# Optimization experiments

Measured on AMD Instinct MI355X. Metric: run time of the kernel, lower is better.

The kernel has to match this reference:

```python
import jax, jax.numpy as jnp
import numpy as np

N_NODES = 50000
N_EDGES = 800000
N_GRAPHS = 512
IN_DIM = 128
HIDDEN = 256
N_CLASSES = 10
MID = 12  # fixed inter-layer dim in TwoConvSAGE


def _segment_mean(x, ids, num_segments):
    s = jax.ops.segment_sum(x, ids, num_segments=num_segments)
    cnt = jax.ops.segment_sum(jnp.ones((x.shape[0],), x.dtype), ids, num_segments=num_segments)
    return jnp.where(cnt[:, None] > 0, s / jnp.maximum(cnt, 1.0)[:, None], 0.0)


def _sage_layer(h, src, dst, Wa, ba, Wb, bb):
    # copy_u + mean: mean over incoming edges of src features
    h_neigh = _segment_mean(h[src], dst, N_NODES)  # [N, d]
    h_total = jnp.concatenate([h, h_neigh], axis=1)  # [N, 2d]
    # nn.Sequential(Linear, Linear) has NO activation in between
    z = (h_total @ Wa + ba) @ Wb + bb
    return jax.nn.relu(z)  # inner F.relu; outer F.relu is idempotent


def setup_inputs() -> dict:
    key = jax.random.key(0)
    ks = jax.random.split(key, 16)
    d = {}
    d['h'] = jax.random.normal(ks[0], (N_NODES, IN_DIM), jnp.float32)
    d['src'] = jax.random.randint(ks[1], (N_EDGES,), 0, N_NODES, jnp.int32)
    d['dst'] = jax.random.randint(ks[2], (N_EDGES,), 0, N_NODES, jnp.int32)
    d['graph_id'] = jnp.sort(jax.random.randint(ks[3], (N_NODES,), 0, N_GRAPHS, jnp.int32))
    s1 = 1.0 / np.sqrt(2 * IN_DIM)
    d['W1a'] = jax.random.uniform(ks[4], (2 * IN_DIM, HIDDEN), jnp.float32, -s1, s1)
    d['b1a'] = jax.random.uniform(ks[5], (HIDDEN,), jnp.float32, -s1, s1)
    s2 = 1.0 / np.sqrt(HIDDEN)
    d['W1b'] = jax.random.uniform(ks[6], (HIDDEN, MID), jnp.float32, -s2, s2)
    d['b1b'] = jax.random.uniform(ks[7], (MID,), jnp.float32, -s2, s2)
    s3 = 1.0 / np.sqrt(2 * MID)
    d['W2a'] = jax.random.uniform(ks[8], (2 * MID, HIDDEN), jnp.float32, -s3, s3)
    d['b2a'] = jax.random.uniform(ks[9], (HIDDEN,), jnp.float32, -s3, s3)
    d['W2b'] = jax.random.uniform(ks[10], (HIDDEN, MID), jnp.float32, -s2, s2)
    d['b2b'] = jax.random.uniform(ks[11], (MID,), jnp.float32, -s2, s2)
    s4 = 1.0 / np.sqrt(MID)
    d['Wc'] = jax.random.uniform(ks[12], (MID, N_CLASSES), jnp.float32, -s4, s4)
    d['bc'] = jax.random.uniform(ks[13], (N_CLASSES,), jnp.float32, -s4, s4)
    return d


def reference(h, src, dst, graph_id, W1a, b1a, W1b, b1b, W2a, b2a, W2b, b2b, Wc, bc):
    h1 = _sage_layer(h, src, dst, W1a, b1a, W1b, b1b)   # [N, 12]
    h2 = _sage_layer(h1, src, dst, W2a, b2a, W2b, b2b)  # [N, 12]
    hg = _segment_mean(h2, graph_id, N_GRAPHS)          # [G, 12]
    return hg @ Wc + bc                                  # [G, n_classes]
```

## Files before the change

### kernel.cpp

```cpp
#include <hip/hip_runtime.h>
#include <hip/hip_bf16.h>

#define NN 50000
#define NE 800000
#define NG 512
#define NB 196
#define B1_CHUNK 2048
#define B1_BLOCKS ((NE + B1_CHUNK - 1) / B1_CHUNK)

typedef unsigned long long ull;

__global__ void prep_kernel(const int* __restrict__ dst, int* __restrict__ hist_mat,
                            const float* __restrict__ W1a, const float* __restrict__ b1a,
                            const float* __restrict__ W1b, const float* __restrict__ b1b,
                            const float* __restrict__ W2a, const float* __restrict__ b2a,
                            const float* __restrict__ W2b, const float* __restrict__ b2b,
                            float* __restrict__ W1eff, float* __restrict__ b1eff,
                            float* __restrict__ W2eff, float* __restrict__ b2eff,
                            const int* __restrict__ gid, int* __restrict__ gstart) {
    int bid = blockIdx.x;
    int tid = threadIdx.x;
    if (bid < B1_BLOCKS) {
        __shared__ int hist[NB];
        for (int i = tid; i < NB; i += 256) hist[i] = 0;
        __syncthreads();
        int e0 = bid * B1_CHUNK;
        #pragma unroll
        for (int k = 0; k < 8; ++k) {
            int e = e0 + tid + k * 256;
            if (e < NE) atomicAdd(&hist[dst[e] >> 8], 1);
        }
        __syncthreads();
        int* row = hist_mat + bid * NB;
        for (int i = tid; i < NB; i += 256) row[i] = hist[i];
    } else if (bid < B1_BLOCKS + 14) {
        int t = (bid - B1_BLOCKS) * 256 + tid;
        if (t < 3072) {
            int r = t / 12, c = t % 12;
            float acc = 0.f;
            for (int k = 0; k < 256; ++k) acc += W1a[r*256 + k] * W1b[k*12 + c];
            W1eff[r*12 + c] = acc;
        } else if (t < 3084) {
            int c = t - 3072;
            float acc = b1b[c];
            for (int k = 0; k < 256; ++k) acc += b1a[k] * W1b[k*12 + c];
            b1eff[c] = acc;
        } else if (t < 3372) {
            int u = t - 3084;
            int r = u / 12, c = u % 12;
            float acc = 0.f;
            for (int k = 0; k < 256; ++k) acc += W2a[r*256 + k] * W2b[k*12 + c];
            W2eff[r*12 + c] = acc;
        } else if (t < 3384) {
            int c = t - 3372;
            float acc = b2b[c];
            for (int k = 0; k < 256; ++k) acc += b2a[k] * W2b[k*12 + c];
            b2eff[c] = acc;
        }
    } else {
        int n = (bid - B1_BLOCKS - 14) * 256 + tid;
        if (n < NN) {
            int cur = gid[n];
            int prev = (n == 0) ? -1 : gid[n - 1];
            for (int g = prev + 1; g <= cur; ++g) gstart[g] = n;
            if (n == NN - 1) {
                for (int g = cur + 1; g <= NG; ++g) gstart[g] = NN;
            }
        }
    }
}

__global__ void offs_kernel(const int* __restrict__ hist_mat,
                            int* __restrict__ off_mat, int* __restrict__ btot) {
    __shared__ int sh[512];
    int tid = threadIdx.x;
    int b = blockIdx.x;
    int v = (tid < B1_BLOCKS) ? hist_mat[tid * NB + b] : 0;
    sh[tid] = v;
    __syncthreads();
    for (int off = 1; off < 512; off <<= 1) {
        int t = (tid >= off) ? sh[tid - off] : 0;
        __syncthreads();
        sh[tid] += t;
        __syncthreads();
    }
    if (tid < B1_BLOCKS) off_mat[tid * NB + b] = sh[tid] - v;
    if (tid == B1_BLOCKS - 1) btot[b] = sh[tid];
}

__global__ void place_pairs_kernel(const int* __restrict__ src, const int* __restrict__ dst,
                                   const int* __restrict__ off_mat, const int* __restrict__ btot,
                                   ull* __restrict__ pairs) {
    __shared__ int sb[256];
    __shared__ int lbase[NB];
    __shared__ int lcur[NB];
    int tid = threadIdx.x;
    int v = (tid < NB) ? btot[tid] : 0;
    sb[tid] = v;
    __syncthreads();
    for (int off = 1; off < 256; off <<= 1) {
        int t = (tid >= off) ? sb[tid - off] : 0;
        __syncthreads();
        sb[tid] += t;
        __syncthreads();
    }
    const int* orow = off_mat + blockIdx.x * NB;
    if (tid < NB) {
        lbase[tid] = (sb[tid] - v) + orow[tid];
        lcur[tid] = 0;
    }
    __syncthreads();
    int e0 = blockIdx.x * B1_CHUNK;
    #pragma unroll
    for (int k = 0; k < 8; ++k) {
        int e = e0 + tid + k * 256;
        if (e < NE) {
            int dd = dst[e];
            int ss = src[e];
            int bb = dd >> 8;
            int idx = atomicAdd(&lcur[bb], 1);
            pairs[lbase[bb] + idx] = ((ull)(unsigned)ss << 32) | (unsigned)dd;
        }
    }
}

__global__ void p1_kernel(const float* __restrict__ h, const float* __restrict__ W1eff,
                          float* __restrict__ p1t, float* __restrict__ p1b) {
    int n = blockIdx.x * blockDim.x + threadIdx.x;
    if (n >= NN) return;
    const float4* hrow = (const float4*)(h + (size_t)n * 128);
    float acc[24];
    #pragma unroll
    for (int j = 0; j < 24; ++j) acc[j] = 0.f;
    #pragma unroll 4
    for (int kq = 0; kq < 32; ++kq) {
        float4 hv = hrow[kq];
        #pragma unroll
        for (int u = 0; u < 4; ++u) {
            int k = kq * 4 + u;
            float hx = u == 0 ? hv.x : (u == 1 ? hv.y : (u == 2 ? hv.z : hv.w));
            const float4* wt = (const float4*)(W1eff + k * 12);
            const float4* wb = (const float4*)(W1eff + (128 + k) * 12);
            #pragma unroll
            for (int q = 0; q < 3; ++q) {
                float4 a = wt[q];
                float4 b = wb[q];
                acc[q*4 + 0]      += hx * a.x;
                acc[q*4 + 1]      += hx * a.y;
                acc[q*4 + 2]      += hx * a.z;
                acc[q*4 + 3]      += hx * a.w;
                acc[12 + q*4 + 0] += hx * b.x;
                acc[12 + q*4 + 1] += hx * b.y;
                acc[12 + q*4 + 2] += hx * b.z;
                acc[12 + q*4 + 3] += hx * b.w;
            }
        }
    }
    float* pt = p1t + (size_t)n * 12;
    float* pb = p1b + (size_t)n * 12;
    #pragma unroll
    for (int c = 0; c < 12; ++c) pt[c] = acc[c];
    #pragma unroll
    for (int c = 0; c < 12; ++c) pb[c] = acc[12 + c];
}

__global__ void fine_gf1_kernel(const ull* __restrict__ pairs, const int* __restrict__ btot,
                                const float* __restrict__ p1t, const float* __restrict__ p1b,
                                const float* __restrict__ b1eff, const float* __restrict__ W2eff,
                                int* __restrict__ row_start, int* __restrict__ sorted_src,
                                float* __restrict__ p2t, float* __restrict__ p2b) {
    __shared__ int sb[256];
    __shared__ int cnt[256];
    __shared__ int sc[256];
    __shared__ int rs[257];
    __shared__ float hacc[256 * 13];
    __shared__ float w2[288];
    __shared__ float b1[12];
    int tid = threadIdx.x;
    int b = blockIdx.x;
    if (tid < 256) { sb[tid] = (tid < NB) ? btot[tid] : 0; cnt[tid] = 0; }
    for (int i = tid; i < 288; i += 768) w2[i] = W2eff[i];
    if (tid >= 256 && tid < 268) b1[tid - 256] = b1eff[tid - 256];
    __syncthreads();
    for (int off = 1; off < 256; off <<= 1) {
        int t = (tid < 256 && tid >= off) ? sb[tid - off] : 0;
        __syncthreads();
        if (tid < 256) sb[tid] += t;
        __syncthreads();
    }
    int vb = btot[b];
    int R0 = sb[b] - vb, R1 = R0 + vb;
    for (int i = R0 + tid; i < R1; i += 768)
        atomicAdd(&cnt[(int)(pairs[i] & 255ULL)], 1);
    __syncthreads();
    if (tid < 256) sc[tid] = cnt[tid];
    __syncthreads();
    for (int off = 1; off < 256; off <<= 1) {
        int t = (tid < 256 && tid >= off) ? sc[tid - off] : 0;
        __syncthreads();
        if (tid < 256) sc[tid] += t;
        __syncthreads();
    }
    if (tid < 256) rs[tid] = R0 + sc[tid] - cnt[tid];
    if (tid == 255) rs[256] = R0 + sc[255];
    __syncthreads();
    if (tid < 256) cnt[tid] = 0;
    int n0 = b << 8;
    int nloc = min(256, NN - n0);
    if (tid < nloc) row_start[n0 + tid] = rs[tid];
    if (b == NB - 1 && tid == 0) row_start[NN] = R1;
    __syncthreads();
    for (int i = R0 + tid; i < R1; i += 768) {
        ull pr = pairs[i];
        int ln = (int)(pr & 255ULL);
        int ss = (int)(pr >> 32);
        int off = atomicAdd(&cnt[ln], 1);
        sorted_src[rs[ln] + off] = ss;
    }
    __syncthreads();
    {
        int li = tid / 3, q = tid - li * 3;
        int r0 = rs[li], r1 = rs[li + 1];
        float4 s = make_float4(0.f, 0.f, 0.f, 0.f);
        for (int i = r0; i < r1; ++i) {
            int sn = sorted_src[i];
            float4 v = ((const float4*)(p1b + (size_t)sn * 12))[q];
            s.x += v.x; s.y += v.y; s.z += v.z; s.w += v.w;
        }
        float* hp = &hacc[li * 13 + q * 4];
        hp[0] = s.x; hp[1] = s.y; hp[2] = s.z; hp[3] = s.w;
    }
    __syncthreads();
    int n = n0 + tid;
    if (tid < 256 && n < NN) {
        int dg = rs[tid + 1] - rs[tid];
        float inv = dg > 0 ? 1.f / (float)dg : 0.f;
        const float4* ptp = (const float4*)(p1t + (size_t)n * 12);
        float4 a0 = ptp[0], a1 = ptp[1], a2 = ptp[2];
        float pt[12] = {a0.x,a0.y,a0.z,a0.w, a1.x,a1.y,a1.z,a1.w, a2.x,a2.y,a2.z,a2.w};
        float h1[12];
        #pragma unroll
        for (int j = 0; j < 12; ++j) {
            float v = pt[j] + hacc[tid * 13 + j] * inv + b1[j];
            h1[j] = v > 0.f ? v : 0.f;
        }
        float oa[12], ob[12];
        #pragma unroll
        for (int co = 0; co < 12; ++co) {
            float A = 0.f, B = 0.f;
            #pragma unroll
            for (int k = 0; k < 12; ++k) {
                A += h1[k] * w2[k*12 + co];
                B += h1[k] * w2[(12+k)*12 + co];
            }
            oa[co] = A; ob[co] = B;
        }
        float4* ot = (float4*)(p2t + (size_t)n * 12);
        float4* ou = (float4*)(p2b + (size_t)n * 12);
        ot[0] = make_float4(oa[0],oa[1],oa[2],oa[3]);
        ot[1] = make_float4(oa[4],oa[5],oa[6],oa[7]);
        ot[2] = make_float4(oa[8],oa[9],oa[10],oa[11]);
        ou[0] = make_float4(ob[0],ob[1],ob[2],ob[3]);
        ou[1] = make_float4(ob[4],ob[5],ob[6],ob[7]);
        ou[2] = make_float4(ob[8],ob[9],ob[10],ob[11]);
    }
}

__global__ void gather_fin2_kernel(const int* __restrict__ row_start, const int* __restrict__ sorted_src,
                                   const float* __restrict__ p2t, const float* __restrict__ p2b,
                                   const float* __restrict__ b2eff, float* __restrict__ h2) {
    int t = blockIdx.x * blockDim.x + threadIdx.x;
    if (t >= NN * 3) return;
    int n = t / 3, q = t - n * 3;
    int r0 = row_start[n], r1 = row_start[n + 1];
    float4 s = make_float4(0.f, 0.f, 0.f, 0.f);
    for (int i = r0; i < r1; ++i) {
        int sn = sorted_src[i];
        float4 v = ((const float4*)(p2b + (size_t)sn * 12))[q];
        s.x += v.x; s.y += v.y; s.z += v.z; s.w += v.w;
    }
    float inv = (r1 > r0) ? 1.f / (float)(r1 - r0) : 0.f;
    float4 pt = ((const float4*)(p2t + (size_t)n * 12))[q];
    const float* b2 = b2eff + q * 4;
    float4 o;
    o.x = pt.x + s.x * inv + b2[0]; o.x = o.x > 0.f ? o.x : 0.f;
    o.y = pt.y + s.y * inv + b2[1]; o.y = o.y > 0.f ? o.y : 0.f;
    o.z = pt.z + s.z * inv + b2[2]; o.z = o.z > 0.f ? o.z : 0.f;
    o.w = pt.w + s.w * inv + b2[3]; o.w = o.w > 0.f ? o.w : 0.f;
    ((float4*)(h2 + (size_t)n * 12))[q] = o;
}

__global__ void graph_kernel(const float* __restrict__ h2, const int* __restrict__ gstart,
                             const float* __restrict__ Wc, const float* __restrict__ bc,
                             float* __restrict__ out) {
    __shared__ float sh[252];
    __shared__ float hg[12];
    int g = blockIdx.x;
    int r0 = gstart[g], r1 = gstart[g + 1];
    int tid = threadIdx.x;
    int group = tid / 12, ch = tid - group * 12;
    if (tid < 252) {
        float s = 0.f;
        for (int n = r0 + group; n < r1; n += 21) s += h2[(size_t)n * 12 + ch];
        sh[tid] = s;
    }
    __syncthreads();
    if (tid < 12) {
        float tot = 0.f;
        #pragma unroll
        for (int k = 0; k < 21; ++k) tot += sh[k*12 + tid];
        int cntn = r1 - r0;
        hg[tid] = cntn > 0 ? tot / (float)cntn : 0.f;
    }
    __syncthreads();
    if (tid < 10) {
        float o = bc[tid];
        #pragma unroll
        for (int j = 0; j < 12; ++j) o += hg[j] * Wc[j*10 + tid];
        out[g*10 + tid] = o;
    }
}

extern "C" void kernel_launch(void* const* d_in, const int* in_sizes, int n_in,
                              void* d_out, int out_size, void* d_ws, size_t ws_size,
                              hipStream_t stream) {
    const float* h   = (const float*)d_in[0];
    const int* src   = (const int*)d_in[1];
    const int* dst   = (const int*)d_in[2];
    const int* gid   = (const int*)d_in[3];
    const float* W1a = (const float*)d_in[4];
    const float* b1a = (const float*)d_in[5];
    const float* W1b = (const float*)d_in[6];
    const float* b1b = (const float*)d_in[7];
    const float* W2a = (const float*)d_in[8];
    const float* b2a = (const float*)d_in[9];
    const float* W2b = (const float*)d_in[10];
    const float* b2b = (const float*)d_in[11];
    const float* Wc  = (const float*)d_in[12];
    const float* bc  = (const float*)d_in[13];
    float* out = (float*)d_out;

    float* ws = (float*)d_ws;
    float* W1eff = ws;
    float* b1eff = ws + 3072;
    float* W2eff = ws + 3084;
    float* b2eff = ws + 3372;
    float* p1t   = ws + 1000000;
    float* p1b   = ws + 1600000;
    float* p2t   = ws + 2200000;
    float* p2b   = ws + 2800000;
    float* h2    = ws + 3400000;
    ull*   pairs = (ull*)(ws + 4000000);
    int*   hist_mat   = (int*)(ws + 5600000);
    int*   off_mat    = (int*)(ws + 5680000);
    int*   sorted_src = (int*)(ws + 5760000);
    int*   row_start  = (int*)(ws + 6560000);
    int*   btot       = (int*)(ws + 6620000);
    int*   gstart     = (int*)(ws + 6624000);

    prep_kernel<<<B1_BLOCKS + 14 + 196, 256, 0, stream>>>(
        dst, hist_mat, W1a, b1a, W1b, b1b, W2a, b2a, W2b, b2b,
        W1eff, b1eff, W2eff, b2eff, gid, gstart);

    offs_kernel<<<NB, 512, 0, stream>>>(hist_mat, off_mat, btot);

    place_pairs_kernel<<<B1_BLOCKS, 256, 0, stream>>>(src, dst, off_mat, btot, pairs);

    p1_kernel<<<(NN + 255) / 256, 256, 0, stream>>>(h, W1eff, p1t, p1b);

    fine_gf1_kernel<<<NB, 768, 0, stream>>>(pairs, btot, p1t, p1b, b1eff, W2eff,
                                            row_start, sorted_src, p2t, p2b);

    gather_fin2_kernel<<<(NN * 3 + 255) / 256, 256, 0, stream>>>(row_start, sorted_src,
                                                                 p2t, p2b, b2eff, h2);

    graph_kernel<<<NG, 256, 0, stream>>>(h2, gstart, Wc, bc, out);
}
```

Measured before the change: 100.1 us.

## Fuse all pipeline stages into one cooperative persistent kernel with grid syncs

The seven separate kernels (prep, offsets, pair placement, p1 projection, fine sort with layer-1 gather, layer-2 gather, graph pooling) are merged into a single cooperative launch of 196 blocks of 768 threads. Stage boundaries become grid.sync calls, and chunked work (edge histograms, pair placement, graph readout) is looped over by the persistent blocks. The goal is to remove per-kernel launch gaps and tail effects between the many short stages. In exchange, every stage runs at a fixed 196-block occupancy, the unified kernel carries the register and shared-memory footprint of the heaviest stage, and each grid-wide barrier has its own cost.

```diff
diff --git a/kernel.cpp b/kernel.cpp
--- a/kernel.cpp
+++ b/kernel.cpp
@@ -1,5 +1,8 @@
 #include <hip/hip_runtime.h>
 #include <hip/hip_bf16.h>
+#include <hip/hip_cooperative_groups.h>
+
+namespace cg = cooperative_groups;
 
 #define NN 50000
 #define NE 800000
@@ -7,34 +10,47 @@
 #define NB 196
 #define B1_CHUNK 2048
 #define B1_BLOCKS ((NE + B1_CHUNK - 1) / B1_CHUNK)
+#define GRID_X 196
+#define BLK 768
 
 typedef unsigned long long ull;
 
-__global__ void prep_kernel(const int* __restrict__ dst, int* __restrict__ hist_mat,
-                            const float* __restrict__ W1a, const float* __restrict__ b1a,
-                            const float* __restrict__ W1b, const float* __restrict__ b1b,
-                            const float* __restrict__ W2a, const float* __restrict__ b2a,
-                            const float* __restrict__ W2b, const float* __restrict__ b2b,
-                            float* __restrict__ W1eff, float* __restrict__ b1eff,
-                            float* __restrict__ W2eff, float* __restrict__ b2eff,
-                            const int* __restrict__ gid, int* __restrict__ gstart) {
-    int bid = blockIdx.x;
-    int tid = threadIdx.x;
-    if (bid < B1_BLOCKS) {
-        __shared__ int hist[NB];
-        for (int i = tid; i < NB; i += 256) hist[i] = 0;
-        __syncthreads();
-        int e0 = bid * B1_CHUNK;
-        #pragma unroll
-        for (int k = 0; k < 8; ++k) {
-            int e = e0 + tid + k * 256;
-            if (e < NE) atomicAdd(&hist[dst[e] >> 8], 1);
-        }
-        __syncthreads();
-        int* row = hist_mat + bid * NB;
-        for (int i = tid; i < NB; i += 256) row[i] = hist[i];
-    } else if (bid < B1_BLOCKS + 14) {
-        int t = (bid - B1_BLOCKS) * 256 + tid;
+__global__ void __launch_bounds__(BLK) mega_kernel(
+    const float* __restrict__ h, const int* __restrict__ src, const int* __restrict__ dst,
+    const int* __restrict__ gid,
+    const float* __restrict__ W1a, const float* __restrict__ b1a,
+    const float* __restrict__ W1b, const float* __restrict__ b1b,
+    const float* __restrict__ W2a, const float* __restrict__ b2a,
+    const float* __restrict__ W2b, const float* __restrict__ b2b,
+    const float* __restrict__ Wc, const float* __restrict__ bc,
+    float* __restrict__ out,
+    float* __restrict__ W1eff, float* __restrict__ b1eff,
+    float* __restrict__ W2eff, float* __restrict__ b2eff,
+    float* __restrict__ p1t, float* __restrict__ p1b,
+    float* __restrict__ p2t, float* __restrict__ p2b, float* __restrict__ h2,
+    ull* __restrict__ pairs, int* __restrict__ hist_mat, int* __restrict__ off_mat,
+    int* __restrict__ sorted_src, int* __restrict__ row_start,
+    int* __restrict__ btot, int* __restrict__ gstart)
+{
+    cg::grid_group grid = cg::this_grid();
+    const int tid = threadIdx.x;
+    const int bid = blockIdx.x;
+    const int gtid = bid * BLK + tid;
+
+    __shared__ int hist[NB];
+    __shared__ int sh512[512];
+    __shared__ int bb[NB];
+    __shared__ int lbase[NB];
+    __shared__ int lcur[NB];
+    __shared__ int cnt[256];
+    __shared__ int sc[256];
+    __shared__ int rs[257];
+    __shared__ float hacc[256 * 13];
+    __shared__ float w2s[288];
+    __shared__ float b1s[12];
+
+    {
+        int t = gtid;
         if (t < 3072) {
             int r = t / 12, c = t % 12;
             float acc = 0.f;
@@ -57,267 +73,241 @@
             for (int k = 0; k < 256; ++k) acc += b2a[k] * W2b[k*12 + c];
             b2eff[c] = acc;
         }
-    } else {
-        int n = (bid - B1_BLOCKS - 14) * 256 + tid;
-        if (n < NN) {
-            int cur = gid[n];
-            int prev = (n == 0) ? -1 : gid[n - 1];
-            for (int g = prev + 1; g <= cur; ++g) gstart[g] = n;
-            if (n == NN - 1) {
-                for (int g = cur + 1; g <= NG; ++g) gstart[g] = NN;
+    }
+    for (int chunk = bid; chunk < B1_BLOCKS; chunk += GRID_X) {
+        for (int i = tid; i < NB; i += BLK) hist[i] = 0;
+        __syncthreads();
+        int e0 = chunk * B1_CHUNK;
+        int e1 = min(e0 + B1_CHUNK, NE);
+        for (int e = e0 + tid; e < e1; e += BLK) atomicAdd(&hist[dst[e] >> 8], 1);
+        __syncthreads();
+        int* row = hist_mat + chunk * NB;
+        for (int i = tid; i < NB; i += BLK) row[i] = hist[i];
+        __syncthreads();
+    }
+    if (gtid < NN) {
+        int n = gtid;
+        int cur = gid[n];
+        int prev = (n == 0) ? -1 : gid[n - 1];
+        for (int g = prev + 1; g <= cur; ++g) gstart[g] = n;
+        if (n == NN - 1) {
+            for (int g = cur + 1; g <= NG; ++g) gstart[g] = NN;
+        }
+    }
+    grid.sync();
+
+    {
+        int b = bid;
+        int v = (tid < B1_BLOCKS) ? hist_mat[tid * NB + b] : 0;
+        if (tid < 512) sh512[tid] = v;
+        __syncthreads();
+        for (int off = 1; off < 512; off <<= 1) {
+            int t2 = (tid < 512 && tid >= off) ? sh512[tid - off] : 0;
+            __syncthreads();
+            if (tid < 512) sh512[tid] += t2;
+            __syncthreads();
+        }
+        if (tid < B1_BLOCKS) off_mat[tid * NB + b] = sh512[tid] - v;
+        if (tid == B1_BLOCKS - 1) btot[b] = sh512[tid];
+    }
+    if (gtid < NN) {
+        int n = gtid;
+        const float4* hrow = (const float4*)(h + (size_t)n * 128);
+        float acc[24];
+        #pragma unroll
+        for (int j = 0; j < 24; ++j) acc[j] = 0.f;
+        #pragma unroll 4
+        for (int kq = 0; kq < 32; ++kq) {
+            float4 hv = hrow[kq];
+            #pragma unroll
+            for (int u = 0; u < 4; ++u) {
+                int k = kq * 4 + u;
+                float hx = u == 0 ? hv.x : (u == 1 ? hv.y : (u == 2 ? hv.z : hv.w));
+                const float4* wt = (const float4*)(W1eff + k * 12);
+                const float4* wb = (const float4*)(W1eff + (128 + k) * 12);
+                #pragma unroll
+                for (int q = 0; q < 3; ++q) {
+                    float4 a = wt[q];
+                    float4 b = wb[q];
+                    acc[q*4 + 0]      += hx * a.x;
+                    acc[q*4 + 1]      += hx * a.y;
+                    acc[q*4 + 2]      += hx * a.z;
+                    acc[q*4 + 3]      += hx * a.w;
+                    acc[12 + q*4 + 0] += hx * b.x;
+                    acc[12 + q*4 + 1] += hx * b.y;
+                    acc[12 + q*4 + 2] += hx * b.z;
+                    acc[12 + q*4 + 3] += hx * b.w;
+                }
             }
         }
-    }
-}
-
-__global__ void offs_kernel(const int* __restrict__ hist_mat,
-                            int* __restrict__ off_mat, int* __restrict__ btot) {
-    __shared__ int sh[512];
-    int tid = threadIdx.x;
-    int b = blockIdx.x;
-    int v = (tid < B1_BLOCKS) ? hist_mat[tid * NB + b] : 0;
-    sh[tid] = v;
+        float* pt = p1t + (size_t)n * 12;
+        float* pb = p1b + (size_t)n * 12;
+        #pragma unroll
+        for (int c = 0; c < 12; ++c) pt[c] = acc[c];
+        #pragma unroll
+        for (int c = 0; c < 12; ++c) pb[c] = acc[12 + c];
+    }
+    grid.sync();
+
+    {
+        int v = (tid < NB) ? btot[tid] : 0;
+        if (tid < 256) sh512[tid] = v;
+        __syncthreads();
+        for (int off = 1; off < 256; off <<= 1) {
+            int t2 = (tid < 256 && tid >= off) ? sh512[tid - off] : 0;
+            __syncthreads();
+            if (tid < 256) sh512[tid] += t2;
+            __syncthreads();
+        }
+        if (tid < NB) bb[tid] = sh512[tid] - v;
+    }
     __syncthreads();
-    for (int off = 1; off < 512; off <<= 1) {
-        int t = (tid >= off) ? sh[tid - off] : 0;
-        __syncthreads();
-        sh[tid] += t;
-        __syncthreads();
-    }
-    if (tid < B1_BLOCKS) off_mat[tid * NB + b] = sh[tid] - v;
-    if (tid == B1_BLOCKS - 1) btot[b] = sh[tid];
-}
-
-__global__ void place_pairs_kernel(const int* __restrict__ src, const int* __restrict__ dst,
-                                   const int* __restrict__ off_mat, const int* __restrict__ btot,
-                                   ull* __restrict__ pairs) {
-    __shared__ int sb[256];
-    __shared__ int lbase[NB];
-    __shared__ int lcur[NB];
-    int tid = threadIdx.x;
-    int v = (tid < NB) ? btot[tid] : 0;
-    sb[tid] = v;
-    __syncthreads();
-    for (int off = 1; off < 256; off <<= 1) {
-        int t = (tid >= off) ? sb[tid - off] : 0;
-        __syncthreads();
-        sb[tid] += t;
-        __syncthreads();
-    }
-    const int* orow = off_mat + blockIdx.x * NB;
-    if (tid < NB) {
-        lbase[tid] = (sb[tid] - v) + orow[tid];
-        lcur[tid] = 0;
-    }
-    __syncthreads();
-    int e0 = blockIdx.x * B1_CHUNK;
-    #pragma unroll
-    for (int k = 0; k < 8; ++k) {
-        int e = e0 + tid + k * 256;
-        if (e < NE) {
+    for (int chunk = bid; chunk < B1_BLOCKS; chunk += GRID_X) {
+        const int* orow = off_mat + chunk * NB;
+        for (int i = tid; i < NB; i += BLK) { lbase[i] = bb[i] + orow[i]; lcur[i] = 0; }
+        __syncthreads();
+        int e0 = chunk * B1_CHUNK;
+        int e1 = min(e0 + B1_CHUNK, NE);
+        for (int e = e0 + tid; e < e1; e += BLK) {
             int dd = dst[e];
             int ss = src[e];
-            int bb = dd >> 8;
-            int idx = atomicAdd(&lcur[bb], 1);
-            pairs[lbase[bb] + idx] = ((ull)(unsigned)ss << 32) | (unsigned)dd;
-        }
-    }
-}
-
-__global__ void p1_kernel(const float* __restrict__ h, const float* __restrict__ W1eff,
-                          float* __restrict__ p1t, float* __restrict__ p1b) {
-    int n = blockIdx.x * blockDim.x + threadIdx.x;
-    if (n >= NN) return;
-    const float4* hrow = (const float4*)(h + (size_t)n * 128);
-    float acc[24];
-    #pragma unroll
-    for (int j = 0; j < 24; ++j) acc[j] = 0.f;
-    #pragma unroll 4
-    for (int kq = 0; kq < 32; ++kq) {
-        float4 hv = hrow[kq];
-        #pragma unroll
-        for (int u = 0; u < 4; ++u) {
-            int k = kq * 4 + u;
-            float hx = u == 0 ? hv.x : (u == 1 ? hv.y : (u == 2 ? hv.z : hv.w));
-            const float4* wt = (const float4*)(W1eff + k * 12);
-            const float4* wb = (const float4*)(W1eff + (128 + k) * 12);
-            #pragma unroll
-            for (int q = 0; q < 3; ++q) {
-                float4 a = wt[q];
-                float4 b = wb[q];
-                acc[q*4 + 0]      += hx * a.x;
-                acc[q*4 + 1]      += hx * a.y;
-                acc[q*4 + 2]      += hx * a.z;
-                acc[q*4 + 3]      += hx * a.w;
-                acc[12 + q*4 + 0] += hx * b.x;
-                acc[12 + q*4 + 1] += hx * b.y;
-                acc[12 + q*4 + 2] += hx * b.z;
-                acc[12 + q*4 + 3] += hx * b.w;
+            int bbk = dd >> 8;
+            int idx = atomicAdd(&lcur[bbk], 1);
+            pairs[lbase[bbk] + idx] = ((ull)(unsigned)ss << 32) | (unsigned)dd;
+        }
+        __syncthreads();
+    }
+    grid.sync();
+
+    {
+        int b = bid;
+        int R0 = bb[b];
+        int R1 = R0 + btot[b];
+        if (tid < 256) cnt[tid] = 0;
+        for (int i = tid; i < 288; i += BLK) w2s[i] = W2eff[i];
+        if (tid < 12) b1s[tid] = b1eff[tid];
+        __syncthreads();
+        for (int i = R0 + tid; i < R1; i += BLK)
+            atomicAdd(&cnt[(int)(pairs[i] & 255ULL)], 1);
+        __syncthreads();
+        if (tid < 256) sc[tid] = cnt[tid];
+        __syncthreads();
+        for (int off = 1; off < 256; off <<= 1) {
+            int t2 = (tid < 256 && tid >= off) ? sc[tid - off] : 0;
+            __syncthreads();
+            if (tid < 256) sc[tid] += t2;
+            __syncthreads();
+        }
+        if (tid < 256) rs[tid] = R0 + sc[tid] - cnt[tid];
+        if (tid == 255) rs[256] = R0 + sc[255];
+        __syncthreads();
+        if (tid < 256) cnt[tid] = 0;
+        int n0 = b << 8;
+        int nloc = min(256, NN - n0);
+        if (tid < nloc) row_start[n0 + tid] = rs[tid];
+        if (b == NB - 1 && tid == 0) row_start[NN] = R1;
+        __syncthreads();
+        for (int i = R0 + tid; i < R1; i += BLK) {
+            ull pr = pairs[i];
+            int ln = (int)(pr & 255ULL);
+            int ss = (int)(pr >> 32);
+            int off2 = atomicAdd(&cnt[ln], 1);
+            sorted_src[rs[ln] + off2] = ss;
+        }
+        __syncthreads();
+        {
+            int li = tid / 3, q = tid - li * 3;
+            int r0 = rs[li], r1 = rs[li + 1];
+            float4 s = make_float4(0.f, 0.f, 0.f, 0.f);
+            for (int i = r0; i < r1; ++i) {
+                int sn = sorted_src[i];
+                float4 v = ((const float4*)(p1b + (size_t)sn * 12))[q];
+                s.x += v.x; s.y += v.y; s.z += v.z; s.w += v.w;
             }
-        }
-    }
-    float* pt = p1t + (size_t)n * 12;
-    float* pb = p1b + (size_t)n * 12;
-    #pragma unroll
-    for (int c = 0; c < 12; ++c) pt[c] = acc[c];
-    #pragma unroll
-    for (int c = 0; c < 12; ++c) pb[c] = acc[12 + c];
-}
-
-__global__ void fine_gf1_kernel(const ull* __restrict__ pairs, const int* __restrict__ btot,
-                                const float* __restrict__ p1t, const float* __restrict__ p1b,
-                                const float* __restrict__ b1eff, const float* __restrict__ W2eff,
-                                int* __restrict__ row_start, int* __restrict__ sorted_src,
-                                float* __restrict__ p2t, float* __restrict__ p2b) {
-    __shared__ int sb[256];
-    __shared__ int cnt[256];
-    __shared__ int sc[256];
-    __shared__ int rs[257];
-    __shared__ float hacc[256 * 13];
-    __shared__ float w2[288];
-    __shared__ float b1[12];
-    int tid = threadIdx.x;
-    int b = blockIdx.x;
-    if (tid < 256) { sb[tid] = (tid < NB) ? btot[tid] : 0; cnt[tid] = 0; }
-    for (int i = tid; i < 288; i += 768) w2[i] = W2eff[i];
-    if (tid >= 256 && tid < 268) b1[tid - 256] = b1eff[tid - 256];
-    __syncthreads();
-    for (int off = 1; off < 256; off <<= 1) {
-        int t = (tid < 256 && tid >= off) ? sb[tid - off] : 0;
-        __syncthreads();
-        if (tid < 256) sb[tid] += t;
-        __syncthreads();
-    }
-    int vb = btot[b];
-    int R0 = sb[b] - vb, R1 = R0 + vb;
-    for (int i = R0 + tid; i < R1; i += 768)
-        atomicAdd(&cnt[(int)(pairs[i] & 255ULL)], 1);
-    __syncthreads();
-    if (tid < 256) sc[tid] = cnt[tid];
-    __syncthreads();
-    for (int off = 1; off < 256; off <<= 1) {
-        int t = (tid < 256 && tid >= off) ? sc[tid - off] : 0;
-        __syncthreads();
-        if (tid < 256) sc[tid] += t;
-        __syncthreads();
-    }
-    if (tid < 256) rs[tid] = R0 + sc[tid] - cnt[tid];
-    if (tid == 255) rs[256] = R0 + sc[255];
-    __syncthreads();
-    if (tid < 256) cnt[tid] = 0;
-    int n0 = b << 8;
-    int nloc = min(256, NN - n0);
-    if (tid < nloc) row_start[n0 + tid] = rs[tid];
-    if (b == NB - 1 && tid == 0) row_start[NN] = R1;
-    __syncthreads();
-    for (int i = R0 + tid; i < R1; i += 768) {
-        ull pr = pairs[i];
-        int ln = (int)(pr & 255ULL);
-        int ss = (int)(pr >> 32);
-        int off = atomicAdd(&cnt[ln], 1);
-        sorted_src[rs[ln] + off] = ss;
-    }
-    __syncthreads();
-    {
-        int li = tid / 3, q = tid - li * 3;
-        int r0 = rs[li], r1 = rs[li + 1];
+            float* hp = &hacc[li * 13 + q * 4];
+            hp[0] = s.x; hp[1] = s.y; hp[2] = s.z; hp[3] = s.w;
+        }
+        __syncthreads();
+        int n = n0 + tid;
+        if (tid < 256 && n < NN) {
+            int dg = rs[tid + 1] - rs[tid];
+            float inv = dg > 0 ? 1.f / (float)dg : 0.f;
+            const float4* ptp = (const float4*)(p1t + (size_t)n * 12);
+            float4 a0 = ptp[0], a1 = ptp[1], a2 = ptp[2];
+            float pt[12] = {a0.x,a0.y,a0.z,a0.w, a1.x,a1.y,a1.z,a1.w, a2.x,a2.y,a2.z,a2.w};
+            float h1[12];
+            #pragma unroll
+            for (int j = 0; j < 12; ++j) {
+                float v = pt[j] + hacc[tid * 13 + j] * inv + b1s[j];
+                h1[j] = v > 0.f ? v : 0.f;
+            }
+            float oa[12], ob[12];
+            #pragma unroll
+            for (int co = 0; co < 12; ++co) {
+                float A = 0.f, B = 0.f;
+                #pragma unroll
+                for (int k = 0; k < 12; ++k) {
+                    A += h1[k] * w2s[k*12 + co];
+                    B += h1[k] * w2s[(12+k)*12 + co];
+                }
+                oa[co] = A; ob[co] = B;
+            }
+            float4* ot = (float4*)(p2t + (size_t)n * 12);
+            float4* ou = (float4*)(p2b + (size_t)n * 12);
+            ot[0] = make_float4(oa[0],oa[1],oa[2],oa[3]);
+            ot[1] = make_float4(oa[4],oa[5],oa[6],oa[7]);
+            ot[2] = make_float4(oa[8],oa[9],oa[10],oa[11]);
+            ou[0] = make_float4(ob[0],ob[1],ob[2],ob[3]);
+            ou[1] = make_float4(ob[4],ob[5],ob[6],ob[7]);
+            ou[2] = make_float4(ob[8],ob[9],ob[10],ob[11]);
+        }
+    }
+    grid.sync();
+
+    if (gtid < NN * 3) {
+        int t = gtid;
+        int n = t / 3, q = t - n * 3;
+        int r0 = row_start[n], r1 = row_start[n + 1];
         float4 s = make_float4(0.f, 0.f, 0.f, 0.f);
         for (int i = r0; i < r1; ++i) {
             int sn = sorted_src[i];
-            float4 v = ((const float4*)(p1b + (size_t)sn * 12))[q];
+            float4 v = ((const float4*)(p2b + (size_t)sn * 12))[q];
             s.x += v.x; s.y += v.y; s.z += v.z; s.w += v.w;
         }
-        float* hp = &hacc[li * 13 + q * 4];
-        hp[0] = s.x; hp[1] = s.y; hp[2] = s.z; hp[3] = s.w;
-    }
-    __syncthreads();
-    int n = n0 + tid;
-    if (tid < 256 && n < NN) {
-        int dg = rs[tid + 1] - rs[tid];
-        float inv = dg > 0 ? 1.f / (float)dg : 0.f;
-        const float4* ptp = (const float4*)(p1t + (size_t)n * 12);
-        float4 a0 = ptp[0], a1 = ptp[1], a2 = ptp[2];
-        float pt[12] = {a0.x,a0.y,a0.z,a0.w, a1.x,a1.y,a1.z,a1.w, a2.x,a2.y,a2.z,a2.w};
-        float h1[12];
-        #pragma unroll
-        for (int j = 0; j < 12; ++j) {
-            float v = pt[j] + hacc[tid * 13 + j] * inv + b1[j];
-            h1[j] = v > 0.f ? v : 0.f;
-        }
-        float oa[12], ob[12];
-        #pragma unroll
-        for (int co = 0; co < 12; ++co) {
-            float A = 0.f, B = 0.f;
-            #pragma unroll
-            for (int k = 0; k < 12; ++k) {
-                A += h1[k] * w2[k*12 + co];
-                B += h1[k] * w2[(12+k)*12 + co];
-            }
-            oa[co] = A; ob[co] = B;
-        }
-        float4* ot = (float4*)(p2t + (size_t)n * 12);
-        float4* ou = (float4*)(p2b + (size_t)n * 12);
-        ot[0] = make_float4(oa[0],oa[1],oa[2],oa[3]);
-        ot[1] = make_float4(oa[4],oa[5],oa[6],oa[7]);
-        ot[2] = make_float4(oa[8],oa[9],oa[10],oa[11]);
-        ou[0] = make_float4(ob[0],ob[1],ob[2],ob[3]);
-        ou[1] = make_float4(ob[4],ob[5],ob[6],ob[7]);
-        ou[2] = make_float4(ob[8],ob[9],ob[10],ob[11]);
-    }
-}
-
-__global__ void gather_fin2_kernel(const int* __restrict__ row_start, const int* __restrict__ sorted_src,
-                                   const float* __restrict__ p2t, const float* __restrict__ p2b,
-                                   const float* __restrict__ b2eff, float* __restrict__ h2) {
-    int t = blockIdx.x * blockDim.x + threadIdx.x;
-    if (t >= NN * 3) return;
-    int n = t / 3, q = t - n * 3;
-    int r0 = row_start[n], r1 = row_start[n + 1];
-    float4 s = make_float4(0.f, 0.f, 0.f, 0.f);
-    for (int i = r0; i < r1; ++i) {
-        int sn = sorted_src[i];
-        float4 v = ((const float4*)(p2b + (size_t)sn * 12))[q];
-        s.x += v.x; s.y += v.y; s.z += v.z; s.w += v.w;
-    }
-    float inv = (r1 > r0) ? 1.f / (float)(r1 - r0) : 0.f;
-    float4 pt = ((const float4*)(p2t + (size_t)n * 12))[q];
-    const float* b2 = b2eff + q * 4;
-    float4 o;
-    o.x = pt.x + s.x * inv + b2[0]; o.x = o.x > 0.f ? o.x : 0.f;
-    o.y = pt.y + s.y * inv + b2[1]; o.y = o.y > 0.f ? o.y : 0.f;
-    o.z = pt.z + s.z * inv + b2[2]; o.z = o.z > 0.f ? o.z : 0.f;
-    o.w = pt.w + s.w * inv + b2[3]; o.w = o.w > 0.f ? o.w : 0.f;
-    ((float4*)(h2 + (size_t)n * 12))[q] = o;
-}
-
-__global__ void graph_kernel(const float* __restrict__ h2, const int* __restrict__ gstart,
-                             const float* __restrict__ Wc, const float* __restrict__ bc,
-                             float* __restrict__ out) {
-    __shared__ float sh[252];
-    __shared__ float hg[12];
-    int g = blockIdx.x;
-    int r0 = gstart[g], r1 = gstart[g + 1];
-    int tid = threadIdx.x;
-    int group = tid / 12, ch = tid - group * 12;
-    if (tid < 252) {
+        float inv = (r1 > r0) ? 1.f / (float)(r1 - r0) : 0.f;
+        float4 pt = ((const float4*)(p2t + (size_t)n * 12))[q];
+        const float* b2 = b2eff + q * 4;
+        float4 o;
+        o.x = pt.x + s.x * inv + b2[0]; o.x = o.x > 0.f ? o.x : 0.f;
+        o.y = pt.y + s.y * inv + b2[1]; o.y = o.y > 0.f ? o.y : 0.f;
+        o.z = pt.z + s.z * inv + b2[2]; o.z = o.z > 0.f ? o.z : 0.f;
+        o.w = pt.w + s.w * inv + b2[3]; o.w = o.w > 0.f ? o.w : 0.f;
+        ((float4*)(h2 + (size_t)n * 12))[q] = o;
+    }
+    grid.sync();
+
+    for (int g = bid; g < NG; g += GRID_X) {
+        int r0 = gstart[g], r1 = gstart[g + 1];
+        int group = tid / 12, ch = tid - group * 12;
         float s = 0.f;
-        for (int n = r0 + group; n < r1; n += 21) s += h2[(size_t)n * 12 + ch];
-        sh[tid] = s;
-    }
-    __syncthreads();
-    if (tid < 12) {
-        float tot = 0.f;
-        #pragma unroll
-        for (int k = 0; k < 21; ++k) tot += sh[k*12 + tid];
-        int cntn = r1 - r0;
-        hg[tid] = cntn > 0 ? tot / (float)cntn : 0.f;
-    }
-    __syncthreads();
-    if (tid < 10) {
-        float o = bc[tid];
-        #pragma unroll
-        for (int j = 0; j < 12; ++j) o += hg[j] * Wc[j*10 + tid];
-        out[g*10 + tid] = o;
+        for (int n = r0 + group; n < r1; n += 64) s += h2[(size_t)n * 12 + ch];
+        hacc[tid] = s;
+        __syncthreads();
+        if (tid < 12) {
+            float tot = 0.f;
+            #pragma unroll
+            for (int k = 0; k < 64; ++k) tot += hacc[k*12 + tid];
+            int cn = r1 - r0;
+            hacc[1024 + tid] = cn > 0 ? tot / (float)cn : 0.f;
+        }
+        __syncthreads();
+        if (tid < 10) {
+            float o = bc[tid];
+            #pragma unroll
+            for (int j = 0; j < 12; ++j) o += hacc[1024 + j] * Wc[j*10 + tid];
+            out[g*10 + tid] = o;
+        }
+        __syncthreads();
     }
 }
 
@@ -358,21 +348,16 @@
     int*   btot       = (int*)(ws + 6620000);
     int*   gstart     = (int*)(ws + 6624000);
 
-    prep_kernel<<<B1_BLOCKS + 14 + 196, 256, 0, stream>>>(
-        dst, hist_mat, W1a, b1a, W1b, b1b, W2a, b2a, W2b, b2b,
-        W1eff, b1eff, W2eff, b2eff, gid, gstart);
-
-    offs_kernel<<<NB, 512, 0, stream>>>(hist_mat, off_mat, btot);
-
-    place_pairs_kernel<<<B1_BLOCKS, 256, 0, stream>>>(src, dst, off_mat, btot, pairs);
-
-    p1_kernel<<<(NN + 255) / 256, 256, 0, stream>>>(h, W1eff, p1t, p1b);
-
-    fine_gf1_kernel<<<NB, 768, 0, stream>>>(pairs, btot, p1t, p1b, b1eff, W2eff,
-                                            row_start, sorted_src, p2t, p2b);
-
-    gather_fin2_kernel<<<(NN * 3 + 255) / 256, 256, 0, stream>>>(row_start, sorted_src,
-                                                                 p2t, p2b, b2eff, h2);
-
-    graph_kernel<<<NG, 256, 0, stream>>>(h2, gstart, Wc, bc, out);
+    void* args[] = {
+        (void*)&h, (void*)&src, (void*)&dst, (void*)&gid,
+        (void*)&W1a, (void*)&b1a, (void*)&W1b, (void*)&b1b,
+        (void*)&W2a, (void*)&b2a, (void*)&W2b, (void*)&b2b,
+        (void*)&Wc, (void*)&bc, (void*)&out,
+        (void*)&W1eff, (void*)&b1eff, (void*)&W2eff, (void*)&b2eff,
+        (void*)&p1t, (void*)&p1b, (void*)&p2t, (void*)&p2b, (void*)&h2,
+        (void*)&pairs, (void*)&hist_mat, (void*)&off_mat,
+        (void*)&sorted_src, (void*)&row_start, (void*)&btot, (void*)&gstart
+    };
+    hipLaunchCooperativeKernel((const void*)mega_kernel, dim3(GRID_X), dim3(BLK),
+                               args, 0, stream);
 }
```

Result: slower. 282.8 us (+182.5%).

## Compress edge pairs to 32-bit, sorted sources to 16-bit, stage CSR in LDS

Applied to the files above, without the earlier changes.

Edge pairs are packed into 32-bit words (source index shifted by 8 bits, plus the low 8 bits of the destination) instead of 64-bit words. The CSR source array is stored as 16-bit indices, which is enough because node ids stay below 65536. In the fused fine-sort kernel, the bucket's sorted sources are also written to an LDS array when the bucket fits in CAP, and the neighbour gather then reads indices from LDS instead of global memory. This cuts global traffic for the pair and index arrays across several kernels. It costs extra shared memory and ties correctness to the node count fitting in 16 bits.

```diff
diff --git a/kernel.cpp b/kernel.cpp
--- a/kernel.cpp
+++ b/kernel.cpp
@@ -7,8 +7,10 @@
 #define NB 196
 #define B1_CHUNK 2048
 #define B1_BLOCKS ((NE + B1_CHUNK - 1) / B1_CHUNK)
-
-typedef unsigned long long ull;
+#define CAP 5120
+
+typedef unsigned int uint32;
+typedef unsigned short ushort16;
 
 __global__ void prep_kernel(const int* __restrict__ dst, int* __restrict__ hist_mat,
                             const float* __restrict__ W1a, const float* __restrict__ b1a,
@@ -90,7 +92,7 @@
 
 __global__ void place_pairs_kernel(const int* __restrict__ src, const int* __restrict__ dst,
                                    const int* __restrict__ off_mat, const int* __restrict__ btot,
-                                   ull* __restrict__ pairs) {
+                                   uint32* __restrict__ pairs) {
     __shared__ int sb[256];
     __shared__ int lbase[NB];
     __shared__ int lcur[NB];
@@ -119,7 +121,7 @@
             int ss = src[e];
             int bb = dd >> 8;
             int idx = atomicAdd(&lcur[bb], 1);
-            pairs[lbase[bb] + idx] = ((ull)(unsigned)ss << 32) | (unsigned)dd;
+            pairs[lbase[bb] + idx] = ((uint32)ss << 8) | (uint32)(dd & 255);
         }
     }
 }
@@ -164,10 +166,10 @@
     for (int c = 0; c < 12; ++c) pb[c] = acc[12 + c];
 }
 
-__global__ void fine_gf1_kernel(const ull* __restrict__ pairs, const int* __restrict__ btot,
+__global__ void fine_gf1_kernel(const uint32* __restrict__ pairs, const int* __restrict__ btot,
                                 const float* __restrict__ p1t, const float* __restrict__ p1b,
                                 const float* __restrict__ b1eff, const float* __restrict__ W2eff,
-                                int* __restrict__ row_start, int* __restrict__ sorted_src,
+                                int* __restrict__ row_start, ushort16* __restrict__ sorted_src,
                                 float* __restrict__ p2t, float* __restrict__ p2b) {
     __shared__ int sb[256];
     __shared__ int cnt[256];
@@ -176,6 +178,7 @@
     __shared__ float hacc[256 * 13];
     __shared__ float w2[288];
     __shared__ float b1[12];
+    __shared__ ushort16 ssrc[CAP];
     int tid = threadIdx.x;
     int b = blockIdx.x;
     if (tid < 256) { sb[tid] = (tid < NB) ? btot[tid] : 0; cnt[tid] = 0; }
@@ -190,8 +193,9 @@
     }
     int vb = btot[b];
     int R0 = sb[b] - vb, R1 = R0 + vb;
+    bool use_lds = (vb <= CAP);
     for (int i = R0 + tid; i < R1; i += 768)
-        atomicAdd(&cnt[(int)(pairs[i] & 255ULL)], 1);
+        atomicAdd(&cnt[(int)(pairs[i] & 255u)], 1);
     __syncthreads();
     if (tid < 256) sc[tid] = cnt[tid];
     __syncthreads();
@@ -211,21 +215,31 @@
     if (b == NB - 1 && tid == 0) row_start[NN] = R1;
     __syncthreads();
     for (int i = R0 + tid; i < R1; i += 768) {
-        ull pr = pairs[i];
-        int ln = (int)(pr & 255ULL);
-        int ss = (int)(pr >> 32);
-        int off = atomicAdd(&cnt[ln], 1);
-        sorted_src[rs[ln] + off] = ss;
+        uint32 pr = pairs[i];
+        int ln = (int)(pr & 255u);
+        int ss = (int)(pr >> 8);
+        int off2 = atomicAdd(&cnt[ln], 1);
+        int pos = rs[ln] + off2;
+        sorted_src[pos] = (ushort16)ss;
+        if (use_lds) ssrc[pos - R0] = (ushort16)ss;
     }
     __syncthreads();
     {
         int li = tid / 3, q = tid - li * 3;
         int r0 = rs[li], r1 = rs[li + 1];
         float4 s = make_float4(0.f, 0.f, 0.f, 0.f);
-        for (int i = r0; i < r1; ++i) {
-            int sn = sorted_src[i];
-            float4 v = ((const float4*)(p1b + (size_t)sn * 12))[q];
-            s.x += v.x; s.y += v.y; s.z += v.z; s.w += v.w;
+        if (use_lds) {
+            for (int i = r0 - R0; i < r1 - R0; ++i) {
+                int sn = (int)ssrc[i];
+                float4 v = ((const float4*)(p1b + (size_t)sn * 12))[q];
+                s.x += v.x; s.y += v.y; s.z += v.z; s.w += v.w;
+            }
+        } else {
+            for (int i = r0; i < r1; ++i) {
+                int sn = (int)sorted_src[i];
+                float4 v = ((const float4*)(p1b + (size_t)sn * 12))[q];
+                s.x += v.x; s.y += v.y; s.z += v.z; s.w += v.w;
+            }
         }
         float* hp = &hacc[li * 13 + q * 4];
         hp[0] = s.x; hp[1] = s.y; hp[2] = s.z; hp[3] = s.w;
@@ -266,7 +280,8 @@
     }
 }
 
-__global__ void gather_fin2_kernel(const int* __restrict__ row_start, const int* __restrict__ sorted_src,
+__global__ void gather_fin2_kernel(const int* __restrict__ row_start,
+                                   const ushort16* __restrict__ sorted_src,
                                    const float* __restrict__ p2t, const float* __restrict__ p2b,
                                    const float* __restrict__ b2eff, float* __restrict__ h2) {
     int t = blockIdx.x * blockDim.x + threadIdx.x;
@@ -275,7 +290,7 @@
     int r0 = row_start[n], r1 = row_start[n + 1];
     float4 s = make_float4(0.f, 0.f, 0.f, 0.f);
     for (int i = r0; i < r1; ++i) {
-        int sn = sorted_src[i];
+        int sn = (int)sorted_src[i];
         float4 v = ((const float4*)(p2b + (size_t)sn * 12))[q];
         s.x += v.x; s.y += v.y; s.z += v.z; s.w += v.w;
     }
@@ -350,13 +365,13 @@
     float* p2t   = ws + 2200000;
     float* p2b   = ws + 2800000;
     float* h2    = ws + 3400000;
-    ull*   pairs = (ull*)(ws + 4000000);
-    int*   hist_mat   = (int*)(ws + 5600000);
-    int*   off_mat    = (int*)(ws + 5680000);
-    int*   sorted_src = (int*)(ws + 5760000);
-    int*   row_start  = (int*)(ws + 6560000);
-    int*   btot       = (int*)(ws + 6620000);
-    int*   gstart     = (int*)(ws + 6624000);
+    uint32* pairs = (uint32*)(ws + 4000000);
+    int*   hist_mat   = (int*)(ws + 4800000);
+    int*   off_mat    = (int*)(ws + 4880000);
+    ushort16* sorted_src = (ushort16*)(ws + 4960000);
+    int*   row_start  = (int*)(ws + 5360000);
+    int*   btot       = (int*)(ws + 5420000);
+    int*   gstart     = (int*)(ws + 5424000);
 
     prep_kernel<<<B1_BLOCKS + 14 + 196, 256, 0, stream>>>(
         dst, hist_mat, W1a, b1a, W1b, b1b, W2a, b2a, W2b, b2b,
```

After: 95.77 us. 4.3% less time.
